# Kernel tuning notes

Hardware: AMD Instinct MI355X
Metric: run time of the kernel (lower is better)

## Reference

```python
import jax, jax.numpy as jnp
import numpy as np

B, N, M = 4, 10000, 10000
P = 128          # num_pts (sampled query points)
K_SAMPLE = 32    # knn_for_sample
K_SCORE = 4      # knn_for_score
Z = 128          # feature dim
SIGMA = 0.01


def setup_inputs() -> dict:
    key = jax.random.key(0)
    ks = jax.random.split(key, 16)
    rn = lambda k, shape, scale: (jax.random.normal(k, shape, dtype=jnp.float32) * scale)
    inp = {
        "noisy_pc": rn(ks[0], (B, N, 3), 1.0),
        "clean_pc": rn(ks[1], (B, M, 3), 1.0),
        "sampled_idx": jax.random.randint(ks[2], (P,), 0, N, dtype=jnp.int32),
        "Wf1": rn(ks[3], (3, 64), 1.0 / np.sqrt(3)),
        "bf1": jnp.zeros((64,), jnp.float32),
        "Wf2": rn(ks[4], (64, Z), 1.0 / np.sqrt(64)),
        "bf2": jnp.zeros((Z,), jnp.float32),
        "Ws1": rn(ks[5], (3 + Z, 128), 1.0 / np.sqrt(3 + Z)),
        "bs1": jnp.zeros((128,), jnp.float32),
        "Ws2": rn(ks[6], (128, 64), 1.0 / np.sqrt(128)),
        "bs2": jnp.zeros((64,), jnp.float32),
        "Ws3": rn(ks[7], (64, 3), 1.0 / np.sqrt(64)),
        "bs3": jnp.zeros((3,), jnp.float32),
    }
    return inp


def _sqdist(q, r):
    # q: (..., Q, 3), r: (..., R, 3) -> (..., Q, R) squared distances
    q2 = jnp.sum(q * q, axis=-1)[..., :, None]
    r2 = jnp.sum(r * r, axis=-1)[..., None, :]
    return q2 + r2 - 2.0 * jnp.matmul(q, jnp.swapaxes(r, -1, -2))


def _knn_gather(q, ref, k):
    # q: (..., Q, 3), ref: (B, R, 3) broadcast-compatible -> nn points (..., Q, k, 3)
    d = _sqdist(q, ref)
    _, idx = jax.lax.top_k(-d, k)          # nearest k (ascending distance)
    return idx


def _forward(noisy_pc, clean_pc, sampled_idx,
             Wf1, bf1, Wf2, bf2, Ws1, bs1, Ws2, bs2, Ws3, bs3):
    # f_origin: sampled query points (B, P, 3)
    f_origin = noisy_pc[:, sampled_idx, :]

    # FeatureExtraction: pointwise MLP over all N points, gather at samples
    feat = jnp.maximum(noisy_pc @ Wf1 + bf1, 0.0) @ Wf2 + bf2      # (B, N, Z)
    noisy_feat = feat[:, sampled_idx, :]                           # (B, P, Z)

    # kNN #1: for each sampled point, K_SAMPLE nearest neighbors in noisy_pc
    idx1 = _knn_gather(f_origin, noisy_pc, K_SAMPLE)               # (B, P, K_SAMPLE)
    f = jax.vmap(lambda pc, i: pc[i])(noisy_pc, idx1)              # (B, P, K_SAMPLE, 3)

    # ScoreNetwork: per-neighbor MLP on [offset, feature]
    x = f - f_origin[:, :, None, :]                                # (B, P, K_SAMPLE, 3)
    z = jnp.broadcast_to(noisy_feat[:, :, None, :], (B, P, K_SAMPLE, Z))
    h = jnp.concatenate([x, z], axis=-1)                           # (B, P, K_SAMPLE, 3+Z)
    h = jnp.maximum(h @ Ws1 + bs1, 0.0)
    h = jnp.maximum(h @ Ws2 + bs2, 0.0)
    estim_score = h @ Ws3 + bs3                                    # (B, P, K_SAMPLE, 3)

    # kNN #2: each neighbor point vs full clean cloud (the hot, huge cdist)
    # dist tensor (B, P, K_SAMPLE, M) computed without materializing the
    # repeated merge_f_origin of the original torch code.
    dot = jnp.einsum("bpkd,bmd->bpkm", f, clean_pc)
    d2 = (jnp.sum(f * f, axis=-1)[..., None]
          + jnp.sum(clean_pc * clean_pc, axis=-1)[:, None, None, :]
          - 2.0 * dot)                                             # (B, P, K_SAMPLE, M)
    _, idx2 = jax.lax.top_k(-d2, K_SCORE)                          # (B, P, K_SAMPLE, K_SCORE)
    nn = jax.vmap(lambda pc, i: pc[i])(clean_pc, idx2)             # (B, P, K_SAMPLE, K_SCORE, 3)

    ground_score = jnp.mean(nn - f[:, :, :, None, :], axis=3)      # (B, P, K_SAMPLE, 3)

    loss = 0.5 * jnp.mean(jnp.sum((estim_score - ground_score) ** 2 * (1.0 / SIGMA), axis=-1))
    return loss


def reference(noisy_pc, clean_pc, sampled_idx,
              Wf1, bf1, Wf2, bf2, Ws1, bs1, Ws2, bs2, Ws3, bs3):
    return _forward(noisy_pc, clean_pc, sampled_idx,
                    Wf1, bf1, Wf2, bf2, Ws1, bs1, Ws2, bs2, Ws3, bs3)
```

## Files before the change

### kernel.cpp

```cpp
#include <hip/hip_runtime.h>

#define BB 4
#define NN 10000
#define MM 10000
#define PP 128
#define KS 32
#define KSC 4
#define ZZ 128

#define OFF_PN 0
#define OFF_PC (OFF_PN + BB*NN*4)
#define OFF_FO (OFF_PC + BB*MM*4)
#define OFF_ZP (OFF_FO + BB*PP*4)
#define OFF_FP (OFF_ZP + BB*PP*ZZ)
#define OFF_GS (OFF_FP + BB*PP*KS*4)
#define OFF_AC (OFF_GS + BB*PP*KS*4)

#define FINF 1e30f

__global__ void k_pack(const float* __restrict__ noisy, const float* __restrict__ clean,
                       float* __restrict__ ws) {
    int t = blockIdx.x * blockDim.x + threadIdx.x;
    if (t == 0) ws[OFF_AC] = 0.0f;
    const int total = BB*NN + BB*MM;
    if (t >= total) return;
    if (t < BB*NN) {
        float x = noisy[t*3+0], y = noisy[t*3+1], z = noisy[t*3+2];
        float w = (x*x + y*y) + z*z;
        ((float4*)(ws + OFF_PN))[t] = make_float4(x, y, z, w);
    } else {
        int u = t - BB*NN;
        float x = clean[u*3+0], y = clean[u*3+1], z = clean[u*3+2];
        float w = -0.5f * ((x*x + y*y) + z*z);
        ((float4*)(ws + OFF_PC))[u] = make_float4(x, y, z, w);
    }
}

__global__ void k_feat(const int* __restrict__ sidx,
                       const float* __restrict__ Wf1, const float* __restrict__ bf1,
                       const float* __restrict__ Wf2, const float* __restrict__ bf2,
                       const float* __restrict__ Ws1, const float* __restrict__ bs1,
                       float* __restrict__ ws) {
    int wave = (blockIdx.x * blockDim.x + threadIdx.x) >> 6;
    int lane = threadIdx.x & 63;
    if (wave >= BB*PP) return;
    int b = wave / PP, p = wave % PP;
    int si = sidx[p];
    float4 q = ((const float4*)(ws + OFF_PN))[b*NN + si];
    if (lane == 0) ((float4*)(ws + OFF_FO))[wave] = q;
    float h = bf1[lane];
    h = fmaf(q.x, Wf1[0*64 + lane], h);
    h = fmaf(q.y, Wf1[1*64 + lane], h);
    h = fmaf(q.z, Wf1[2*64 + lane], h);
    h = fmaxf(h, 0.0f);
    float fa = bf2[lane], fb = bf2[64 + lane];
    for (int i = 0; i < 64; ++i) {
        float hi = __shfl(h, i);
        fa = fmaf(hi, Wf2[i*ZZ + lane],      fa);
        fb = fmaf(hi, Wf2[i*ZZ + 64 + lane], fb);
    }
    float za = bs1[lane], zb = bs1[64 + lane];
    for (int i = 0; i < 64; ++i) {
        float va = __shfl(fa, i);
        float vb = __shfl(fb, i);
        za = fmaf(va, Ws1[(3 + i)*128 + lane],       za);
        zb = fmaf(va, Ws1[(3 + i)*128 + 64 + lane],  zb);
        za = fmaf(vb, Ws1[(67 + i)*128 + lane],      za);
        zb = fmaf(vb, Ws1[(67 + i)*128 + 64 + lane], zb);
    }
    ws[OFF_ZP + wave*ZZ + lane]      = za;
    ws[OFF_ZP + wave*ZZ + 64 + lane] = zb;
}

#define CAP1 512
__global__ __launch_bounds__(256) void k_knn1(const int* __restrict__ sidx, float* __restrict__ ws) {
    __shared__ float cd[CAP1];
    __shared__ int   ci[CAP1];
    __shared__ float wtau[4];
    __shared__ int   cnt;
    int blk = blockIdx.x;
    int b = blk >> 7, p = blk & 127;
    int tid = threadIdx.x;
    int w = tid >> 6, lane = tid & 63;
    const float4* pts = ((const float4*)(ws + OFF_PN)) + b*NN;
    float4 q = pts[sidx[p]];
    if (tid == 0) cnt = 0;
    float t0 = FINF, t1 = FINF;
    for (int j = tid; j < NN; j += 256) {
        float4 r = pts[j];
        float dot = fmaf(q.z, r.z, fmaf(q.y, r.y, q.x*r.x));
        float d = fmaf(dot, -2.0f, q.w + r.w);
        t1 = fminf(t1, fmaxf(t0, d));
        t0 = fminf(t0, d);
    }
    float m = 0.0f;
    for (int r = 0; r < KS; ++r) {
        m = t0;
        m = fminf(m, __shfl_xor(m, 1));
        m = fminf(m, __shfl_xor(m, 2));
        m = fminf(m, __shfl_xor(m, 4));
        m = fminf(m, __shfl_xor(m, 8));
        m = fminf(m, __shfl_xor(m, 16));
        m = fminf(m, __shfl_xor(m, 32));
        if (t0 == m) { t0 = t1; t1 = FINF; }
    }
    if (lane == 0) wtau[w] = m;
    __syncthreads();
    float tau = fminf(fminf(wtau[0], wtau[1]), fminf(wtau[2], wtau[3]));
    for (int j = tid; j < NN; j += 256) {
        float4 r = pts[j];
        float dot = fmaf(q.z, r.z, fmaf(q.y, r.y, q.x*r.x));
        float d = fmaf(dot, -2.0f, q.w + r.w);
        if (d <= tau) {
            int pos = atomicAdd(&cnt, 1);
            if (pos < CAP1) { cd[pos] = d; ci[pos] = j; }
        }
    }
    __syncthreads();
    int C = cnt; if (C > CAP1) C = CAP1;
    for (int i = tid; i < C; i += 256) {
        float di = cd[i]; int ii = ci[i];
        int rank = 0;
        for (int j2 = 0; j2 < C; ++j2) {
            float dj = cd[j2]; int ij = ci[j2];
            rank += ((dj < di) || (dj == di && ij < ii)) ? 1 : 0;
        }
        if (rank < KS) ((float4*)(ws + OFF_FP))[blk*KS + rank] = pts[ii];
    }
}

#define CHK2 1000
#define NCH2 10
#define QPB 32
#define CAP2 128

#define K2Q(c) float fxv##c, fyv##c, fzv##c, tauv##c; \
    float ta0##c = -FINF, ta1##c = -FINF;

#define K2LOAD(c) { float4 f4_ = ((const float4*)(ws + OFF_FP))[qbase + qg*4 + c]; \
    fxv##c = f4_.x; fyv##c = f4_.y; fzv##c = f4_.z; }

#define AUPD(c, R) { float e_ = fmaf(fzv##c,(R).z,fmaf(fyv##c,(R).y,fmaf(fxv##c,(R).x,(R).w))); \
    ta1##c = fmaxf(ta1##c, fminf(ta0##c, e_)); ta0##c = fmaxf(ta0##c, e_); }

#define ASCAN(BUF) \
    for (int t_ = 0; t_ < 16; ++t_) { \
        if (t_ < 15 || sub < 5) { \
            float4 r_ = sp[BUF][sbase + t_*8 + sub]; \
            AUPD(0, r_) AUPD(1, r_) AUPD(2, r_) AUPD(3, r_) \
        } }

#define AMRG(c) { \
    float h0_ = ta0##c, h1_ = ta1##c; \
    _Pragma("unroll") \
    for (int r_ = 0; r_ < 4; ++r_) { \
        float m_ = h0_; \
        m_ = fmaxf(m_, __shfl_xor(m_, 1)); \
        m_ = fmaxf(m_, __shfl_xor(m_, 2)); \
        m_ = fmaxf(m_, __shfl_xor(m_, 4)); \
        if (h0_ == m_) { h0_ = h1_; h1_ = -FINF; } \
        if (sub == r_) sWA[qg*4 + c][w*4 + r_] = m_; \
    } }

#define EVC(c, R) float ev##c = fmaf(fzv##c,(R).z,fmaf(fyv##c,(R).y,fmaf(fxv##c,(R).x,(R).w)));

#define APP(c) if (ev##c >= tauv##c) { \
    int pos_ = atomicAdd(&sCnt[qg*4 + c], 1); \
    if (pos_ < CAP2) { sCE[qg*4 + c][pos_] = ev##c; sCI[qg*4 + c][pos_] = gj_; } }

#define BSCAN(BUF, BASE) \
    for (int t_ = 0; t_ < 16; ++t_) { \
        if (t_ < 15 || sub < 5) { \
            int loc_ = sbase + t_*8 + sub; \
            float4 r_ = sp[BUF][loc_]; \
            EVC(0, r_) EVC(1, r_) EVC(2, r_) EVC(3, r_) \
            float mx_ = fmaxf(fmaxf(ev0, ev1), fmaxf(ev2, ev3)); \
            if (mx_ >= cmin) { \
                int gj_ = (BASE) + loc_; \
                APP(0) APP(1) APP(2) APP(3) \
            } \
        } }

#define STAGE(BUF, CHUNK) \
    for (int u_ = tid; u_ < CHK2; u_ += 512) sp[BUF][u_] = pts[(CHUNK)*CHK2 + u_];

__global__ __launch_bounds__(512) void k_knn2(float* __restrict__ ws) {
    __shared__ float4 sp[2][CHK2];
    __shared__ float  sWA[QPB][33];
    __shared__ float  sCE[QPB][CAP2 + 1];
    __shared__ int    sCI[QPB][CAP2 + 1];
    __shared__ float  sTau[QPB];
    __shared__ int    sCnt[QPB];
    __shared__ int    sTop[QPB][4];
    int tid  = threadIdx.x;
    int w    = tid >> 6;
    int lane = tid & 63;
    int sub  = lane & 7;
    int qg   = lane >> 3;
    int qbase = blockIdx.x * QPB;
    int b = qbase >> 12;
    int sbase = w * 125;
    const float4* pts = ((const float4*)(ws + OFF_PC)) + b*MM;

    K2Q(0) K2Q(1) K2Q(2) K2Q(3)
    K2LOAD(0) K2LOAD(1) K2LOAD(2) K2LOAD(3)
    if (tid < QPB) sCnt[tid] = 0;

    STAGE(0, 0)
    __syncthreads();
    STAGE(1, 1)

    ASCAN(0)
    __syncthreads();
    ASCAN(1)
    AMRG(0) AMRG(1) AMRG(2) AMRG(3)
    __syncthreads();
    if (tid < QPB) {
        float b0 = -FINF, b1 = -FINF, b2 = -FINF, b3 = -FINF;
        #pragma unroll
        for (int u = 0; u < 32; ++u) {
            float v = sWA[tid][u];
            b3 = fmaxf(b3, fminf(b2, v));
            b2 = fmaxf(b2, fminf(b1, v));
            b1 = fmaxf(b1, fminf(b0, v));
            b0 = fmaxf(b0, v);
        }
        sTau[tid] = b3;
    }
    __syncthreads();
    tauv0 = sTau[qg*4 + 0]; tauv1 = sTau[qg*4 + 1];
    tauv2 = sTau[qg*4 + 2]; tauv3 = sTau[qg*4 + 3];
    float cmin = fminf(fminf(tauv0, tauv1), fminf(tauv2, tauv3));

    BSCAN(0, 0)
    __syncthreads();
    STAGE(0, 2) BSCAN(1, 1*CHK2)
    __syncthreads();
    STAGE(1, 3) BSCAN(0, 2*CHK2)
    __syncthreads();
    STAGE(0, 4) BSCAN(1, 3*CHK2)
    __syncthreads();
    STAGE(1, 5) BSCAN(0, 4*CHK2)
    __syncthreads();
    STAGE(0, 6) BSCAN(1, 5*CHK2)
    __syncthreads();
    STAGE(1, 7) BSCAN(0, 6*CHK2)
    __syncthreads();
    STAGE(0, 8) BSCAN(1, 7*CHK2)
    __syncthreads();
    STAGE(1, 9) BSCAN(0, 8*CHK2)
    __syncthreads();
    BSCAN(1, 9*CHK2)
    __syncthreads();

    {
        int qi = tid >> 4;
        int sl = tid & 15;
        int C = sCnt[qi]; if (C > CAP2) C = CAP2;
        for (int i = sl; i < C; i += 16) {
            float ei = sCE[qi][i]; int ii = sCI[qi][i];
            int rank = 0;
            for (int j = 0; j < C; ++j) {
                float ej = sCE[qi][j]; int ij = sCI[qi][j];
                rank += ((ej > ei) || (ej == ei && ij < ii)) ? 1 : 0;
            }
            if (rank < KSC) sTop[qi][rank] = ii;
        }
    }
    __syncthreads();
    if (tid < QPB) {
        int q = qbase + tid;
        float4 f4 = ((const float4*)(ws + OFF_FP))[q];
        float4 n0 = pts[sTop[tid][0]], n1 = pts[sTop[tid][1]];
        float4 n2 = pts[sTop[tid][2]], n3 = pts[sTop[tid][3]];
        float gx = 0.f, gy = 0.f, gz = 0.f;
        gx += n0.x - f4.x; gy += n0.y - f4.y; gz += n0.z - f4.z;
        gx += n1.x - f4.x; gy += n1.y - f4.y; gz += n1.z - f4.z;
        gx += n2.x - f4.x; gy += n2.y - f4.y; gz += n2.z - f4.z;
        gx += n3.x - f4.x; gy += n3.y - f4.y; gz += n3.z - f4.z;
        float* gsp = ws + OFF_GS + (size_t)q*4;
        gsp[0] = gx*0.25f; gsp[1] = gy*0.25f; gsp[2] = gz*0.25f;
    }
}

__global__ __launch_bounds__(256) void k_mlp(const float* __restrict__ Ws1,
                                             const float* __restrict__ Ws2, const float* __restrict__ bs2,
                                             const float* __restrict__ Ws3, const float* __restrict__ bs3,
                                             float* __restrict__ ws) {
    __shared__ float4 sG[2][128];
    __shared__ float4 sW2[128][16];
    __shared__ float  sB2[64];
    __shared__ float  sW3[64][3];
    __shared__ float  sB3[3];
    __shared__ float  sE[3][4][64];
    int tid = threadIdx.x;
    int w = tid >> 6, lane = tid & 63;
    for (int u = tid; u < 2048; u += 256) ((float4*)sW2)[u] = ((const float4*)Ws2)[u];
    if (tid < 64) sB2[tid] = bs2[tid];
    if (tid < 192) ((float*)sW3)[tid] = Ws3[tid];
    if (tid < 3) sB3[tid] = bs3[tid];
    {
        int grp = tid >> 7, i = tid & 127;
        sG[grp][i] = make_float4(ws[OFF_ZP + (blockIdx.x*2 + grp)*ZZ + i],
                                 Ws1[i], Ws1[128 + i], Ws1[256 + i]);
    }
    __syncthreads();

    int g = blockIdx.x*64 + lane;
    float4 f4 = ((const float4*)(ws + OFF_FP))[g];
    float4 fo = ((const float4*)(ws + OFF_FO))[g >> 5];
    float x0 = f4.x - fo.x, x1 = f4.y - fo.y, x2 = f4.z - fo.z;
    int grp = lane >> 5;

    float4 a[4];
    #pragma unroll
    for (int qq = 0; qq < 4; ++qq) a[qq] = make_float4(0.f, 0.f, 0.f, 0.f);
    for (int i = 0; i < 128; ++i) {
        float4 gv = sG[grp][i];
        float h1 = fmaf(x2, gv.w, fmaf(x1, gv.z, fmaf(x0, gv.y, gv.x)));
        h1 = fmaxf(h1, 0.0f);
        #pragma unroll
        for (int qq = 0; qq < 4; ++qq) {
            float4 wv = sW2[i][w*4 + qq];
            a[qq].x = fmaf(h1, wv.x, a[qq].x);
            a[qq].y = fmaf(h1, wv.y, a[qq].y);
            a[qq].z = fmaf(h1, wv.z, a[qq].z);
            a[qq].w = fmaf(h1, wv.w, a[qq].w);
        }
    }
    float p0 = 0.f, p1 = 0.f, p2 = 0.f;
    #pragma unroll
    for (int qq = 0; qq < 4; ++qq) {
        float av[4] = {a[qq].x, a[qq].y, a[qq].z, a[qq].w};
        #pragma unroll
        for (int cc = 0; cc < 4; ++cc) {
            int j = w*16 + qq*4 + cc;
            float h2 = fmaxf(av[cc] + sB2[j], 0.0f);
            p0 = fmaf(h2, sW3[j][0], p0);
            p1 = fmaf(h2, sW3[j][1], p1);
            p2 = fmaf(h2, sW3[j][2], p2);
        }
    }
    sE[0][w][lane] = p0; sE[1][w][lane] = p1; sE[2][w][lane] = p2;
    __syncthreads();
    if (w == 0) {
        float ee0 = ((sE[0][0][lane] + sE[0][1][lane]) + sE[0][2][lane]) + sE[0][3][lane] + sB3[0];
        float ee1 = ((sE[1][0][lane] + sE[1][1][lane]) + sE[1][2][lane]) + sE[1][3][lane] + sB3[1];
        float ee2 = ((sE[2][0][lane] + sE[2][1][lane]) + sE[2][2][lane]) + sE[2][3][lane] + sB3[2];
        const float* gsp = ws + OFF_GS + (size_t)g*4;
        float d0 = ee0 - gsp[0], d1 = ee1 - gsp[1], d2 = ee2 - gsp[2];
        float t = ((d0*d0 + d1*d1) + d2*d2) * 100.0f;
        for (int off = 32; off > 0; off >>= 1) t += __shfl_down(t, off);
        if (lane == 0) atomicAdd(ws + OFF_AC, t);
    }
}

__global__ void k_fin(const float* __restrict__ ws, float* __restrict__ out) {
    if (threadIdx.x == 0 && blockIdx.x == 0)
        out[0] = ws[OFF_AC] * (1.0f / 32768.0f);
}

extern "C" void kernel_launch(void* const* d_in, const int* in_sizes, int n_in,
                              void* d_out, int out_size, void* d_ws, size_t ws_size,
                              hipStream_t stream) {
    const float* noisy = (const float*)d_in[0];
    const float* clean = (const float*)d_in[1];
    const int*   sidx  = (const int*)  d_in[2];
    const float* Wf1 = (const float*)d_in[3];
    const float* bf1 = (const float*)d_in[4];
    const float* Wf2 = (const float*)d_in[5];
    const float* bf2 = (const float*)d_in[6];
    const float* Ws1 = (const float*)d_in[7];
    const float* bs1 = (const float*)d_in[8];
    const float* Ws2 = (const float*)d_in[9];
    const float* bs2 = (const float*)d_in[10];
    const float* Ws3 = (const float*)d_in[11];
    const float* bs3 = (const float*)d_in[12];
    float* ws  = (float*)d_ws;
    float* out = (float*)d_out;

    k_pack<<<(BB*NN + BB*MM + 255)/256, 256, 0, stream>>>(noisy, clean, ws);
    k_feat<<<(BB*PP*64)/256, 256, 0, stream>>>(sidx, Wf1, bf1, Wf2, bf2, Ws1, bs1, ws);
    k_knn1<<<BB*PP, 256, 0, stream>>>(sidx, ws);
    k_knn2<<<(BB*PP*KS)/QPB, 512, 0, stream>>>(ws);
    k_mlp<<<(BB*PP*KS)/64, 256, 0, stream>>>(Ws1, Ws2, bs2, Ws3, bs3, ws);
    k_fin<<<1, 64, 0, stream>>>(ws, out);
}
```

Before: 220.9 us.

## Read clean points directly from global memory in knn2 instead of LDS staging

Removes the double-buffered shared-memory staging of clean-cloud chunks and the per-chunk block barriers in k_knn2. Each wave now reads float4 points straight from global memory (relying on L1/L2 caching) for both the threshold pass over the first 2000 points and the full candidate scan, with two loads in flight per loop iteration. This frees LDS and drops about ten __syncthreads, at the cost of more global/cache traffic and load latency that is no longer hidden by the explicit staging. The point-to-thread assignment also changes from contiguous per-wave slices to strided groups of 8.

After: 234.7 us. 6.3% more time.

```diff
diff --git a/kernel.cpp b/kernel.cpp
--- a/kernel.cpp
+++ b/kernel.cpp
@@ -129,8 +129,6 @@
     }
 }
 
-#define CHK2 1000
-#define NCH2 10
 #define QPB 32
 #define CAP2 128
 
@@ -142,13 +140,6 @@
 
 #define AUPD(c, R) { float e_ = fmaf(fzv##c,(R).z,fmaf(fyv##c,(R).y,fmaf(fxv##c,(R).x,(R).w))); \
     ta1##c = fmaxf(ta1##c, fminf(ta0##c, e_)); ta0##c = fmaxf(ta0##c, e_); }
-
-#define ASCAN(BUF) \
-    for (int t_ = 0; t_ < 16; ++t_) { \
-        if (t_ < 15 || sub < 5) { \
-            float4 r_ = sp[BUF][sbase + t_*8 + sub]; \
-            AUPD(0, r_) AUPD(1, r_) AUPD(2, r_) AUPD(3, r_) \
-        } }
 
 #define AMRG(c) { \
     float h0_ = ta0##c, h1_ = ta1##c; \
@@ -168,24 +159,15 @@
     int pos_ = atomicAdd(&sCnt[qg*4 + c], 1); \
     if (pos_ < CAP2) { sCE[qg*4 + c][pos_] = ev##c; sCI[qg*4 + c][pos_] = gj_; } }
 
-#define BSCAN(BUF, BASE) \
-    for (int t_ = 0; t_ < 16; ++t_) { \
-        if (t_ < 15 || sub < 5) { \
-            int loc_ = sbase + t_*8 + sub; \
-            float4 r_ = sp[BUF][loc_]; \
-            EVC(0, r_) EVC(1, r_) EVC(2, r_) EVC(3, r_) \
-            float mx_ = fmaxf(fmaxf(ev0, ev1), fmaxf(ev2, ev3)); \
-            if (mx_ >= cmin) { \
-                int gj_ = (BASE) + loc_; \
-                APP(0) APP(1) APP(2) APP(3) \
-            } \
-        } }
-
-#define STAGE(BUF, CHUNK) \
-    for (int u_ = tid; u_ < CHK2; u_ += 512) sp[BUF][u_] = pts[(CHUNK)*CHK2 + u_];
+#define PROC1(RV, GJ) { \
+    EVC(0, RV) EVC(1, RV) EVC(2, RV) EVC(3, RV) \
+    float mx_ = fmaxf(fmaxf(ev0, ev1), fmaxf(ev2, ev3)); \
+    if (mx_ >= cmin) { \
+        int gj_ = (GJ); \
+        APP(0) APP(1) APP(2) APP(3) \
+    } }
 
 __global__ __launch_bounds__(512) void k_knn2(float* __restrict__ ws) {
-    __shared__ float4 sp[2][CHK2];
     __shared__ float  sWA[QPB][33];
     __shared__ float  sCE[QPB][CAP2 + 1];
     __shared__ int    sCI[QPB][CAP2 + 1];
@@ -199,20 +181,16 @@
     int qg   = lane >> 3;
     int qbase = blockIdx.x * QPB;
     int b = qbase >> 12;
-    int sbase = w * 125;
     const float4* pts = ((const float4*)(ws + OFF_PC)) + b*MM;
 
     K2Q(0) K2Q(1) K2Q(2) K2Q(3)
     K2LOAD(0) K2LOAD(1) K2LOAD(2) K2LOAD(3)
     if (tid < QPB) sCnt[tid] = 0;
 
-    STAGE(0, 0)
-    __syncthreads();
-    STAGE(1, 1)
-
-    ASCAN(0)
-    __syncthreads();
-    ASCAN(1)
+    for (int g = w; g < 250; g += 8) {
+        float4 r_ = pts[g*8 + sub];
+        AUPD(0, r_) AUPD(1, r_) AUPD(2, r_) AUPD(3, r_)
+    }
     AMRG(0) AMRG(1) AMRG(2) AMRG(3)
     __syncthreads();
     if (tid < QPB) {
@@ -232,25 +210,19 @@
     tauv2 = sTau[qg*4 + 2]; tauv3 = sTau[qg*4 + 3];
     float cmin = fminf(fminf(tauv0, tauv1), fminf(tauv2, tauv3));
 
-    BSCAN(0, 0)
-    __syncthreads();
-    STAGE(0, 2) BSCAN(1, 1*CHK2)
-    __syncthreads();
-    STAGE(1, 3) BSCAN(0, 2*CHK2)
-    __syncthreads();
-    STAGE(0, 4) BSCAN(1, 3*CHK2)
-    __syncthreads();
-    STAGE(1, 5) BSCAN(0, 4*CHK2)
-    __syncthreads();
-    STAGE(0, 6) BSCAN(1, 5*CHK2)
-    __syncthreads();
-    STAGE(1, 7) BSCAN(0, 6*CHK2)
-    __syncthreads();
-    STAGE(0, 8) BSCAN(1, 7*CHK2)
-    __syncthreads();
-    STAGE(1, 9) BSCAN(0, 8*CHK2)
-    __syncthreads();
-    BSCAN(1, 9*CHK2)
+    {
+        int g = w;
+        for (; g + 8 < 1250; g += 16) {
+            float4 r0 = pts[g*8 + sub];
+            float4 r1 = pts[(g+8)*8 + sub];
+            PROC1(r0, g*8 + sub)
+            PROC1(r1, (g+8)*8 + sub)
+        }
+        for (; g < 1250; g += 8) {
+            float4 r0 = pts[g*8 + sub];
+            PROC1(r0, g*8 + sub)
+        }
+    }
     __syncthreads();
 
     {
```
